# Kernel tuning notes

Hardware: AMD Instinct MI355X
Metric: run time of the kernel (lower is better)

Reference implementation:

```python
import jax, jax.numpy as jnp
import numpy as np

N_NODES = 100000
N_EDGES = 3200000
D = 32


def _gat(x, edge_index, W, att_s, att_d, bias, heads, ch, neg_slope):
    """PyG-style GATConv (shared lin for src/dst, add_self_loops=False).
    x: [N, D_in], edge_index: [2, E], W: [heads*ch, D_in],
    att_s/att_d: [heads, ch], bias: [heads*ch]. Returns [N, heads*ch]."""
    n = x.shape[0]
    h = (x @ W.T).reshape(n, heads, ch)                      # [N,H,C]
    a_s = (h * att_s[None]).sum(-1)                           # [N,H]
    a_d = (h * att_d[None]).sum(-1)                           # [N,H]
    src, dst = edge_index[0], edge_index[1]
    logits = jax.nn.leaky_relu(a_s[src] + a_d[dst], neg_slope)  # [E,H]
    # segment softmax over edges grouped by destination node
    m = jax.ops.segment_max(logits, dst, num_segments=n)     # [N,H]
    m = jnp.where(jnp.isfinite(m), m, 0.0)                    # nodes w/ no in-edges
    ex = jnp.exp(logits - m[dst])                             # [E,H]
    denom = jax.ops.segment_sum(ex, dst, num_segments=n)     # [N,H]
    alpha = ex / (denom[dst] + 1e-16)                         # [E,H]
    out = jax.ops.segment_sum(alpha[:, :, None] * h[src], dst, num_segments=n)  # [N,H,C]
    return out.reshape(n, heads * ch) + bias


def setup_inputs() -> dict:
    key = jax.random.key(0)
    ks = jax.random.split(key, 16)
    x = jax.random.normal(ks[0], (N_NODES, D), dtype=jnp.float32)
    edge_index = jax.random.randint(ks[1], (2, N_EDGES), 0, N_NODES, dtype=jnp.int64)
    s = 1.0 / np.sqrt(D)
    return {
        "x": x,
        "edge_index": edge_index,
        "W1": jax.random.normal(ks[2], (32, D), dtype=jnp.float32) * s,
        "att_s1": jax.random.normal(ks[3], (2, 16), dtype=jnp.float32) * 0.05,
        "att_d1": jax.random.normal(ks[4], (2, 16), dtype=jnp.float32) * 0.05,
        "b1": jnp.full((32,), 0.1, dtype=jnp.float32),
        "ea1": jnp.ones((1,), dtype=jnp.float32),  # edge_activator
        "W2": jax.random.normal(ks[5], (32, 32), dtype=jnp.float32) * s,
        "att_s2": jax.random.normal(ks[6], (2, 16), dtype=jnp.float32) * 0.05,
        "att_d2": jax.random.normal(ks[7], (2, 16), dtype=jnp.float32) * 0.05,
        "b2": jnp.full((32,), 0.1, dtype=jnp.float32),
        "W3": jax.random.normal(ks[8], (32, 32), dtype=jnp.float32) * s,
        "att_s3": jax.random.normal(ks[9], (1, 32), dtype=jnp.float32) * 0.05,
        "att_d3": jax.random.normal(ks[10], (1, 32), dtype=jnp.float32) * 0.05,
        "b3": jnp.full((32,), 0.1, dtype=jnp.float32),
    }


def reference(x, edge_index, W1, att_s1, att_d1, b1, ea1,
              W2, att_s2, att_d2, b2, W3, att_s3, att_d3, b3):
    # --- layer 1 (negative_slope=0.01) ---
    h = _gat(x, edge_index, W1, att_s1, att_d1, b1, heads=2, ch=16, neg_slope=0.01)
    scale = jnp.tanh(ea1)[0]
    scale = jnp.where(scale < 0.1, 1.0, scale)  # 'continue' branch skips the scaling
    h = h * scale
    h = h + 0.05 * jax.lax.stop_gradient(h)      # h + 0.05*h.detach()
    h = jax.nn.elu(h)                            # eval path (training=False)
    h = jnp.clip(h, -3.0, 3.0)
    # --- layer 2 (default negative_slope=0.2) ---
    h = _gat(h, edge_index, W2, att_s2, att_d2, b2, heads=2, ch=16, neg_slope=0.2)
    h = jax.nn.elu(h)
    h = jnp.clip(h, -3.0, 3.0)
    # --- layer 3: heads=1, concat=False ---
    out = _gat(h, edge_index, W3, att_s3, att_d3, b3, heads=1, ch=32, neg_slope=0.2)
    return out
```

## Files before the change

### kernel.cpp

```cpp
#include <hip/hip_runtime.h>
#include <hip/hip_bf16.h>
#include <hip/hip_fp16.h>


#define NPB  128
#define CAPB 6144
#define PAD_SENTINEL 0xFFFFFFFFu

__global__ void k_initcur(int* __restrict__ cursor, int nb) {
    int i = blockIdx.x * 256 + threadIdx.x;
    if (i < nb) cursor[i] = i * CAPB;
}

__global__ void __launch_bounds__(1024)
k_bin(const int* __restrict__ src, const int* __restrict__ dst,
      int* __restrict__ bucket_cursor, unsigned int* __restrict__ pairs,
      int e, int nb) {
    const int EPT = 8;
    __shared__ int h[1024];
    __shared__ int cbase[1024];
    __shared__ int room[1024];
    int t = threadIdx.x;
    for (int i = t; i < nb; i += 1024) h[i] = 0;
    __syncthreads();
    int e4 = e >> 2;
    int base4 = blockIdx.x * 2048;
    int boff[EPT];
    unsigned int pk[EPT];
#pragma unroll
    for (int k = 0; k < 2; k++) {
        int i4 = base4 + k * 1024 + t;
        if (i4 < e4) {
            int4 dv = ((const int4*)dst)[i4];
            int4 sv = ((const int4*)src)[i4];
            const int* dd = (const int*)&dv;
            const int* ss = (const int*)&sv;
#pragma unroll
            for (int j = 0; j < 4; j++) {
                int q = 4 * k + j;
                int d = dd[j];
                int b = d >> 7;
                pk[q] = ((unsigned int)ss[j] << 7) | (unsigned int)(d & 127);
                int off = atomicAdd(&h[b], 1);
                boff[q] = (b << 16) | off;
            }
        } else {
#pragma unroll
            for (int j = 0; j < 4; j++) boff[4 * k + j] = -1;
        }
    }
    __syncthreads();
    for (int i = t; i < nb; i += 1024) {
        int c = h[i];
        if (c) {
            int r = (c + 7) & ~7;
            int cb = atomicAdd(&bucket_cursor[i], r);
            int rm = (i + 1) * CAPB - cb;
            cbase[i] = cb;
            room[i] = rm;
            for (int j = c; j < r && j < rm; j++)
                pairs[cb + j] = PAD_SENTINEL;
        }
    }
    __syncthreads();
#pragma unroll
    for (int q = 0; q < EPT; q++) {
        if (boff[q] >= 0) {
            int b = boff[q] >> 16;
            int off = boff[q] & 0xFFFF;
            if (off < room[b]) pairs[cbase[b] + off] = pk[q];
        }
    }
    if (blockIdx.x == 0 && t < (e & 3)) {
        int i = (e & ~3) + t;
        int d = dst[i];
        int b = d >> 7;
        int pos = atomicAdd(&bucket_cursor[b], 1);
        if (pos < (b + 1) * CAPB)
            pairs[pos] = ((unsigned int)src[i] << 7) | (unsigned int)(d & 127);
    }
}

__global__ void __launch_bounds__(512)
k_bucket_sort(const unsigned int* __restrict__ pairs,
              const int* __restrict__ bucket_cursor,
              int2* __restrict__ rowinfo, int* __restrict__ src_sorted,
              int n) {
    __shared__ int cnt[NPB];
    __shared__ int cur[NPB];
    __shared__ int total;
    __shared__ unsigned int lp[CAPB];
    __shared__ int op[CAPB];
    int b = blockIdx.x;
    int t = threadIdx.x;
    int bbase = b * CAPB;
    int m = bucket_cursor[b] - bbase;
    if (m > CAPB) m = CAPB;
    if (t < NPB) cnt[t] = 0;
    __syncthreads();
    for (int cb = 0; cb < m; cb += 4096) {
        unsigned int pv[8];
#pragma unroll
        for (int u = 0; u < 8; u++) {
            int i = cb + u * 512 + t;
            pv[u] = (i < m) ? pairs[bbase + i] : PAD_SENTINEL;
        }
#pragma unroll
        for (int u = 0; u < 8; u++) {
            int i = cb + u * 512 + t;
            if (i < m) lp[i] = pv[u];
            if (pv[u] != PAD_SENTINEL) atomicAdd(&cnt[pv[u] & 127], 1);
        }
    }
    __syncthreads();
    if (t < 64) {
        int c0 = cnt[2 * t];
        int c1 = cnt[2 * t + 1];
        int sum = c0 + c1;
        int run = sum;
#pragma unroll
        for (int off = 1; off < 64; off <<= 1) {
            int v = __shfl_up(run, off, 64);
            if (t >= off) run += v;
        }
        int ex = run - sum;
        cur[2 * t] = ex;
        cur[2 * t + 1] = ex + c0;
        int node = b * NPB + 2 * t;
        if (node < n) rowinfo[node] = make_int2(bbase + ex, c0);
        if (node + 1 < n) rowinfo[node + 1] = make_int2(bbase + ex + c0, c1);
        if (t == 63) total = run;
    }
    __syncthreads();
    for (int cb = 0; cb < m; cb += 4096) {
        unsigned int pv[8];
        int of[8];
#pragma unroll
        for (int u = 0; u < 8; u++) {
            int i = cb + u * 512 + t;
            pv[u] = (i < m) ? lp[i] : PAD_SENTINEL;
        }
#pragma unroll
        for (int u = 0; u < 8; u++)
            if (pv[u] != PAD_SENTINEL) of[u] = atomicAdd(&cur[pv[u] & 127], 1);
#pragma unroll
        for (int u = 0; u < 8; u++)
            if (pv[u] != PAD_SENTINEL) op[of[u]] = (int)(pv[u] >> 7);
    }
    __syncthreads();
    int nt4 = (total + 3) >> 2;
    int4* dst4 = (int4*)(src_sorted + bbase);
    const int4* src4 = (const int4*)op;
    for (int i = t; i < nt4; i += 512) dst4[i] = src4[i];
}

template <int H>
__global__ void k_transform(const float* __restrict__ in, const float* __restrict__ W,
                            const float* __restrict__ att_s, const float* __restrict__ att_d,
                            __half* __restrict__ h16, float* __restrict__ a_s,
                            float* __restrict__ a_d, int n) {
    constexpr int C = 32 / H;
    __shared__ float Wl[32][33];
    __shared__ float xs[8][32];
    int t = threadIdx.x;
    for (int i = t; i < 1024; i += 256) Wl[i >> 5][i & 31] = W[i];
    int nl = t >> 5, o = t & 31;
    int node = blockIdx.x * 8 + nl;
    xs[nl][o] = (node < n) ? in[node * 32 + o] : 0.f;
    __syncthreads();
    float acc = 0.f;
#pragma unroll
    for (int k = 0; k < 32; k++) acc = fmaf(xs[nl][k], Wl[o][k], acc);
    if (node < n) {
        h16[node * 32 + o] = __float2half_rn(acc);
        float vs = acc * att_s[o];
        float vd = acc * att_d[o];
#pragma unroll
        for (int m = C / 2; m >= 1; m >>= 1) {
            vs += __shfl_xor(vs, m, 64);
            vd += __shfl_xor(vd, m, 64);
        }
        if ((o % C) == 0) {
            int hh = o / C;
            a_s[node * H + hh] = vs;
            a_d[node * H + hh] = vd;
        }
    }
}

template <int H, int EPI>
__global__ void k_edge(const int2* __restrict__ rowinfo, const int* __restrict__ src_sorted,
                       const __half* __restrict__ h16,
                       const float* __restrict__ a_s, const float* __restrict__ a_d,
                       const float* __restrict__ bias, const float* __restrict__ ea,
                       float* __restrict__ out, int n, float slope) {
    constexpr int CAP = 128;
    constexpr int RSTR = 2 * CAP + 16;
    __shared__ int lds_raw[8][H][RSTR];
    int nw = threadIdx.x >> 5;
    int hl = threadIdx.x & 31;
    int node = blockIdx.x * 8 + nw;
    if (node >= n) return;
    int2 bi = rowinfo[node];
    int beg = bi.x, deg = bi.y;
    int padB = (deg + 15) & ~15;

    float ad[H];
#pragma unroll
    for (int hh = 0; hh < H; hh++) ad[hh] = a_d[node * H + hh];

    float ds[H];
#pragma unroll
    for (int hh = 0; hh < H; hh++) ds[hh] = 0.f;
    bool fast = (padB <= CAP);
    if (fast) {
        for (int idx = hl; idx < padB; idx += 32) {
            if (idx < deg) {
                int s = src_sorted[beg + idx];
                if (H == 2) {
                    float2 as2 = *(const float2*)((const char*)a_s + (unsigned)(s << 3));
                    float l0 = as2.x + ad[0]; l0 = fmaxf(l0, l0 * slope);
                    float l1 = as2.y + ad[1]; l1 = fmaxf(l1, l1 * slope);
                    float e0 = __expf(l0), e1 = __expf(l1);
                    ds[0] += e0; ds[1] += e1;
                    ((int2*)lds_raw[nw][0])[idx] = make_int2(s, __float_as_int(e0));
                    ((int2*)lds_raw[nw][H - 1])[idx] = make_int2(s, __float_as_int(e1));
                } else {
                    float l0 = a_s[s] + ad[0]; l0 = fmaxf(l0, l0 * slope);
                    float e0 = __expf(l0);
                    ds[0] += e0;
                    ((int2*)lds_raw[nw][0])[idx] = make_int2(s, __float_as_int(e0));
                }
            } else {
#pragma unroll
                for (int hh = 0; hh < H; hh++)
                    ((int2*)lds_raw[nw][hh])[idx] = make_int2(0, 0);
            }
        }
    } else {
        for (int idx = hl; idx < deg; idx += 32) {
            int s = src_sorted[beg + idx];
            if (H == 2) {
                float2 as2 = *(const float2*)((const char*)a_s + (unsigned)(s << 3));
                float l0 = as2.x + ad[0]; l0 = fmaxf(l0, l0 * slope);
                float l1 = as2.y + ad[1]; l1 = fmaxf(l1, l1 * slope);
                ds[0] += __expf(l0); ds[1] += __expf(l1);
            } else {
                float l0 = a_s[s] + ad[0]; l0 = fmaxf(l0, l0 * slope);
                ds[0] += __expf(l0);
            }
        }
    }

    int e2 = hl >> 4;
    int l16 = hl & 15;
    int hd = (H == 2) ? (l16 >> 3) : 0;
    int co = l16 << 2;
    float adh = ad[hd];
    float acc0 = 0.f, acc1 = 0.f;
    const char* hbase = (const char*)h16;
    const int* lb = &lds_raw[nw][hd][e2 * 4];

    if (fast) {
        for (int base = 0; base < padB; base += 16) {
            int4 qa = *(const int4*)(lb + base * 2);
            int4 qb = *(const int4*)(lb + base * 2 + 8);
            int4 qc = *(const int4*)(lb + base * 2 + 16);
            int4 qd = *(const int4*)(lb + base * 2 + 24);
            __half2 h0 = *(const __half2*)(hbase + (unsigned)((qa.x << 6) + co));
            __half2 h1 = *(const __half2*)(hbase + (unsigned)((qa.z << 6) + co));
            __half2 h2 = *(const __half2*)(hbase + (unsigned)((qb.x << 6) + co));
            __half2 h3 = *(const __half2*)(hbase + (unsigned)((qb.z << 6) + co));
            __half2 h4 = *(const __half2*)(hbase + (unsigned)((qc.x << 6) + co));
            __half2 h5 = *(const __half2*)(hbase + (unsigned)((qc.z << 6) + co));
            __half2 h6 = *(const __half2*)(hbase + (unsigned)((qd.x << 6) + co));
            __half2 h7 = *(const __half2*)(hbase + (unsigned)((qd.z << 6) + co));
            float xa0 = __int_as_float(qa.y), xa1 = __int_as_float(qa.w);
            float xb0 = __int_as_float(qb.y), xb1 = __int_as_float(qb.w);
            float xc0 = __int_as_float(qc.y), xc1 = __int_as_float(qc.w);
            float xd0 = __int_as_float(qd.y), xd1 = __int_as_float(qd.w);
            acc0 = fmaf(xa0, __half2float(__low2half(h0)), acc0);
            acc1 = fmaf(xa0, __half2float(__high2half(h0)), acc1);
            acc0 = fmaf(xa1, __half2float(__low2half(h1)), acc0);
            acc1 = fmaf(xa1, __half2float(__high2half(h1)), acc1);
            acc0 = fmaf(xb0, __half2float(__low2half(h2)), acc0);
            acc1 = fmaf(xb0, __half2float(__high2half(h2)), acc1);
            acc0 = fmaf(xb1, __half2float(__low2half(h3)), acc0);
            acc1 = fmaf(xb1, __half2float(__high2half(h3)), acc1);
            acc0 = fmaf(xc0, __half2float(__low2half(h4)), acc0);
            acc1 = fmaf(xc0, __half2float(__high2half(h4)), acc1);
            acc0 = fmaf(xc1, __half2float(__low2half(h5)), acc0);
            acc1 = fmaf(xc1, __half2float(__high2half(h5)), acc1);
            acc0 = fmaf(xd0, __half2float(__low2half(h6)), acc0);
            acc1 = fmaf(xd0, __half2float(__high2half(h6)), acc1);
            acc0 = fmaf(xd1, __half2float(__low2half(h7)), acc0);
            acc1 = fmaf(xd1, __half2float(__high2half(h7)), acc1);
        }
    } else {
        for (int base = 0; base < deg; base += 16) {
#pragma unroll
            for (int u = 0; u < 8; u++) {
                int idx = base + u * 2 + e2;
                int s = 0;
                float ex = 0.f;
                if (idx < deg) {
                    s = src_sorted[beg + idx];
                    float l = a_s[s * H + hd] + adh;
                    l = fmaxf(l, l * slope);
                    ex = __expf(l);
                }
                __half2 hv = *(const __half2*)(hbase + (unsigned)((s << 6) + co));
                acc0 = fmaf(ex, __half2float(__low2half(hv)), acc0);
                acc1 = fmaf(ex, __half2float(__high2half(hv)), acc1);
            }
        }
    }

#pragma unroll
    for (int hh = 0; hh < H; hh++) {
        float v = ds[hh];
#pragma unroll
        for (int m = 16; m >= 1; m >>= 1) v += __shfl_xor(v, m, 64);
        ds[hh] = 1.f / (v + 1e-16f);
    }

    acc0 += __shfl_xor(acc0, 16, 64);
    acc1 += __shfl_xor(acc1, 16, 64);

    if (l16 == hl) {
        float invd = ds[hd];
        float2 bv = *(const float2*)(bias + l16 * 2);
        float v0 = fmaf(acc0, invd, bv.x);
        float v1 = fmaf(acc1, invd, bv.y);
        if (EPI == 1) {
            float s0 = tanhf(ea[0]);
            if (s0 < 0.1f) s0 = 1.0f;
            s0 *= 1.05f;
            v0 *= s0; v1 *= s0;
            v0 = (v0 > 0.f) ? v0 : expm1f(v0);
            v1 = (v1 > 0.f) ? v1 : expm1f(v1);
            v0 = fminf(3.f, fmaxf(-3.f, v0));
            v1 = fminf(3.f, fmaxf(-3.f, v1));
        } else if (EPI == 2) {
            v0 = (v0 > 0.f) ? v0 : expm1f(v0);
            v1 = (v1 > 0.f) ? v1 : expm1f(v1);
            v0 = fminf(3.f, fmaxf(-3.f, v0));
            v1 = fminf(3.f, fmaxf(-3.f, v1));
        }
        *(float2*)(out + (size_t)node * 32 + l16 * 2) = make_float2(v0, v1);
    }
}

extern "C" void kernel_launch(void* const* d_in, const int* in_sizes, int n_in,
                              void* d_out, int out_size, void* d_ws, size_t ws_size,
                              hipStream_t stream) {
    const float* x   = (const float*)d_in[0];
    const int*   ei  = (const int*)d_in[1];
    const float* W1  = (const float*)d_in[2];
    const float* as1 = (const float*)d_in[3];
    const float* ad1 = (const float*)d_in[4];
    const float* b1  = (const float*)d_in[5];
    const float* ea1 = (const float*)d_in[6];
    const float* W2  = (const float*)d_in[7];
    const float* as2 = (const float*)d_in[8];
    const float* ad2 = (const float*)d_in[9];
    const float* b2  = (const float*)d_in[10];
    const float* W3  = (const float*)d_in[11];
    const float* as3 = (const float*)d_in[12];
    const float* ad3 = (const float*)d_in[13];
    const float* b3  = (const float*)d_in[14];
    float* out = (float*)d_out;

    const int n = in_sizes[0] / 32;
    const int e = in_sizes[1] / 2;
    const int* src = ei;
    const int* dst = ei + e;
    const int nb = (n + NPB - 1) / NPB;

    char* w = (char*)d_ws;
    auto alloc = [&](size_t bytes) -> void* {
        void* p = (void*)w;
        w += (bytes + 255) & ~(size_t)255;
        return p;
    };
    __half* h16     = (__half*)alloc((size_t)n * 32 * 2);
    float* a_s      = (float*)alloc((size_t)n * 2 * 4);
    float* a_d      = (float*)alloc((size_t)n * 2 * 4);
    float* bufA     = (float*)alloc((size_t)n * 32 * 4);
    float* bufB     = (float*)alloc((size_t)n * 32 * 4);
    int2* rowinfo   = (int2*)alloc((size_t)n * 8);
    int* bucket_cur = (int*)alloc((size_t)(nb + 1) * 4);
    int* src_sorted = (int*)alloc((size_t)nb * CAPB * 4);
    unsigned int* pairs = (unsigned int*)bufA;

    k_initcur<<<(nb + 255) / 256, 256, 0, stream>>>(bucket_cur, nb);
    int e4 = e >> 2;
    k_bin<<<(e4 + 2047) / 2048, 1024, 0, stream>>>(src, dst, bucket_cur, pairs, e, nb);
    k_bucket_sort<<<nb, 512, 0, stream>>>(pairs, bucket_cur, rowinfo, src_sorted, n);

    const int tgrid = (n + 7) / 8;
    const int egrid = (n + 7) / 8;

    k_transform<2><<<tgrid, 256, 0, stream>>>(x, W1, as1, ad1, h16, a_s, a_d, n);
    k_edge<2, 1><<<egrid, 256, 0, stream>>>(rowinfo, src_sorted, h16, a_s, a_d, b1, ea1, bufA, n, 0.01f);

    k_transform<2><<<tgrid, 256, 0, stream>>>(bufA, W2, as2, ad2, h16, a_s, a_d, n);
    k_edge<2, 2><<<egrid, 256, 0, stream>>>(rowinfo, src_sorted, h16, a_s, a_d, b2, nullptr, bufB, n, 0.2f);

    k_transform<1><<<tgrid, 256, 0, stream>>>(bufB, W3, as3, ad3, h16, a_s, a_d, n);
    k_edge<1, 0><<<egrid, 256, 0, stream>>>(rowinfo, src_sorted, h16, a_s, a_d, b3, nullptr, out, n, 0.2f);
}
```

Before: 341.3 us.

## Stage binned edges in shared memory for coalesced bucket writes

k_bin now prefix-sums per-bucket counts within the block, scatters packed edges into a shared-memory staging buffer ordered by bucket, then has each wavefront copy whole bucket runs to global memory contiguously. This replaces scattered per-edge global stores and the sentinel padding to multiples of 8. Bucket cursors become relative offsets cleared with hipMemsetAsync instead of an init kernel. It adds 32KB of LDS per block, which may lower occupancy. It also assumes nb fits within the 1024-entry shared arrays (the per-bucket cursor atomics are done only by threads 128 and up, so only the first 896 buckets are handled).

```diff
diff --git a/kernel.cpp b/kernel.cpp
--- a/kernel.cpp
+++ b/kernel.cpp
@@ -6,27 +6,22 @@
 #define NPB  128
 #define CAPB 6144
 #define PAD_SENTINEL 0xFFFFFFFFu
-
-__global__ void k_initcur(int* __restrict__ cursor, int nb) {
-    int i = blockIdx.x * 256 + threadIdx.x;
-    if (i < nb) cursor[i] = i * CAPB;
-}
 
 __global__ void __launch_bounds__(1024)
 k_bin(const int* __restrict__ src, const int* __restrict__ dst,
       int* __restrict__ bucket_cursor, unsigned int* __restrict__ pairs,
       int e, int nb) {
-    const int EPT = 8;
     __shared__ int h[1024];
-    __shared__ int cbase[1024];
-    __shared__ int room[1024];
+    __shared__ int bs[1024];
+    __shared__ int cb[1024];
+    __shared__ unsigned int stage[8192];
     int t = threadIdx.x;
-    for (int i = t; i < nb; i += 1024) h[i] = 0;
+    h[t] = 0;
     __syncthreads();
     int e4 = e >> 2;
     int base4 = blockIdx.x * 2048;
-    int boff[EPT];
-    unsigned int pk[EPT];
+    int boff[8];
+    unsigned int pk[8];
 #pragma unroll
     for (int k = 0; k < 2; k++) {
         int i4 = base4 + k * 1024 + t;
@@ -50,34 +45,57 @@
         }
     }
     __syncthreads();
-    for (int i = t; i < nb; i += 1024) {
-        int c = h[i];
-        if (c) {
-            int r = (c + 7) & ~7;
-            int cb = atomicAdd(&bucket_cursor[i], r);
-            int rm = (i + 1) * CAPB - cb;
-            cbase[i] = cb;
-            room[i] = rm;
-            for (int j = c; j < r && j < rm; j++)
-                pairs[cb + j] = PAD_SENTINEL;
-        }
-    }
-    __syncthreads();
-#pragma unroll
-    for (int q = 0; q < EPT; q++) {
+    if (t >= 128 && t - 128 < nb) {
+        int b = t - 128;
+        int c = h[b];
+        cb[b] = c ? atomicAdd(&bucket_cursor[b], c) : 0;
+    }
+    if (t < 64) {
+        int sum = 0;
+#pragma unroll
+        for (int j = 0; j < 16; j++) sum += h[t * 16 + j];
+        int run = sum;
+#pragma unroll
+        for (int off = 1; off < 64; off <<= 1) {
+            int v = __shfl_up(run, off, 64);
+            if (t >= off) run += v;
+        }
+        int base = run - sum;
+#pragma unroll
+        for (int j = 0; j < 16; j++) {
+            int b = t * 16 + j;
+            bs[b] = base;
+            base += h[b];
+        }
+    }
+    __syncthreads();
+#pragma unroll
+    for (int q = 0; q < 8; q++) {
         if (boff[q] >= 0) {
             int b = boff[q] >> 16;
-            int off = boff[q] & 0xFFFF;
-            if (off < room[b]) pairs[cbase[b] + off] = pk[q];
-        }
+            stage[bs[b] + (boff[q] & 0xFFFF)] = pk[q];
+        }
+    }
+    __syncthreads();
+    int wv = t >> 6, ln = t & 63;
+    for (int b = wv; b < nb; b += 16) {
+        int c = h[b];
+        if (c == 0) continue;
+        int gb = cb[b];
+        int room = CAPB - gb;
+        if (c > room) c = (room > 0) ? room : 0;
+        unsigned int* dp = pairs + (size_t)b * CAPB + gb;
+        const unsigned int* sp = stage + bs[b];
+        for (int o = ln; o < c; o += 64) dp[o] = sp[o];
     }
     if (blockIdx.x == 0 && t < (e & 3)) {
         int i = (e & ~3) + t;
         int d = dst[i];
         int b = d >> 7;
-        int pos = atomicAdd(&bucket_cursor[b], 1);
-        if (pos < (b + 1) * CAPB)
-            pairs[pos] = ((unsigned int)src[i] << 7) | (unsigned int)(d & 127);
+        int r = atomicAdd(&bucket_cursor[b], 1);
+        if (r < CAPB)
+            pairs[(size_t)b * CAPB + r] =
+                ((unsigned int)src[i] << 7) | (unsigned int)(d & 127);
     }
 }
 
@@ -94,7 +112,7 @@
     int b = blockIdx.x;
     int t = threadIdx.x;
     int bbase = b * CAPB;
-    int m = bucket_cursor[b] - bbase;
+    int m = bucket_cursor[b];
     if (m > CAPB) m = CAPB;
     if (t < NPB) cnt[t] = 0;
     __syncthreads();
@@ -393,7 +411,7 @@
     int* src_sorted = (int*)alloc((size_t)nb * CAPB * 4);
     unsigned int* pairs = (unsigned int*)bufA;
 
-    k_initcur<<<(nb + 255) / 256, 256, 0, stream>>>(bucket_cur, nb);
+    hipMemsetAsync(bucket_cur, 0, (size_t)nb * 4, stream);
     int e4 = e >> 2;
     k_bin<<<(e4 + 2047) / 2048, 1024, 0, stream>>>(src, dst, bucket_cur, pairs, e, nb);
     k_bucket_sort<<<nb, 512, 0, stream>>>(pairs, bucket_cur, rowinfo, src_sorted, n);
```

New measurement: 341.8 us. Within noise of the previous version (+0.1%).
